# Kernel tuning notes

Hardware: AMD Instinct MI355X
Metric: run time of the kernel (lower is better)

Reference implementation:

```python
import jax, jax.numpy as jnp
import numpy as np


def setup_inputs() -> dict:
    key = jax.random.key(0)
    ks = jax.random.split(key, 7)
    B, T, U = 8, 200, 50
    D_enc, D_dec, J, V = 512, 512, 512, 1024
    s = 0.05
    return {
        "h_enc": jax.random.normal(ks[0], (B, T, 1, D_enc), dtype=jnp.float32),
        "h_dec": jax.random.normal(ks[1], (B, 1, U, D_dec), dtype=jnp.float32),
        "W_enc": jax.random.normal(ks[2], (J, D_enc), dtype=jnp.float32) * s,
        "b_enc": jax.random.normal(ks[3], (J,), dtype=jnp.float32) * s,
        "W_dec": jax.random.normal(ks[4], (J, D_dec), dtype=jnp.float32) * s,
        "W_out": jax.random.normal(ks[5], (V, J), dtype=jnp.float32) * s,
        "b_out": jax.random.normal(ks[6], (V,), dtype=jnp.float32) * s,
    }


def reference(h_enc, h_dec, W_enc, b_enc, W_dec, W_out, b_out):
    # lin_enc: (B,T,1,D_enc) -> (B,T,1,J) ; lin_dec (no bias): (B,1,U,D_dec) -> (B,1,U,J)
    e = jnp.einsum("btod,jd->btoj", h_enc, W_enc) + b_enc
    d = jnp.einsum("boud,jd->bouj", h_dec, W_dec)
    # broadcast add -> (B,T,U,J), Tanh activation
    z = jnp.tanh(e + d)
    # lin_out: (B,T,U,J) -> (B,T,U,V)
    return jnp.einsum("btuj,vj->btuv", z, W_out) + b_out
```

## Files before the change

### kernel.cpp

```cpp
#include <hip/hip_runtime.h>
#include <hip/hip_bf16.h>


typedef short bf16x8 __attribute__((ext_vector_type(8)));
typedef float fx4 __attribute__((ext_vector_type(4)));

static constexpr int KD = 512;
static constexpr int V = 1024;
static constexpr int M_BIG = 80000;

__device__ inline unsigned short f2bf(float f) {
    union { float f; unsigned u; } v; v.f = f;
    unsigned r = v.u + 0x7fffu + ((v.u >> 16) & 1u);
    return (unsigned short)(r >> 16);
}
__device__ inline float bf2f(unsigned short h) {
    union { float f; unsigned u; } v; v.u = ((unsigned)h) << 16; return v.f;
}
__device__ inline float fast_tanh(float x) {
    float p = __builtin_amdgcn_exp2f(x * 2.885390081777926f);
    return 1.0f - 2.0f * __builtin_amdgcn_rcpf(p + 1.0f);
}
__device__ inline void gld_lds16(const void* g, void* l) {
    __builtin_amdgcn_global_load_lds(
        (const __attribute__((address_space(1))) void*)g,
        (__attribute__((address_space(3))) void*)l, 16, 0, 0);
}

__global__ __launch_bounds__(256) void gemm_ed(
    const float* __restrict__ A, const float* __restrict__ W,
    const float* __restrict__ bias, float* __restrict__ out, int Mrows) {
    __shared__ unsigned short As[64 * 32];
    __shared__ unsigned short Ws[64 * 32];
    const int t = threadIdx.x;
    const int lane = t & 63, wid = t >> 6;
    const int m0 = blockIdx.x * 64, n0 = blockIdx.y * 64;
    const int wm = (wid & 1) * 32, wn = (wid >> 1) * 32;

    fx4 acc[2][2];
    const fx4 z4 = {0.f, 0.f, 0.f, 0.f};
    acc[0][0] = z4; acc[0][1] = z4; acc[1][0] = z4; acc[1][1] = z4;

    const int sr = t >> 2;
    const int skc = (t & 3) * 8;
    const int ar = (m0 + sr < Mrows) ? (m0 + sr) : (Mrows - 1);
    const float* Ap = A + (size_t)ar * KD + skc;
    const float* Wp = W + (size_t)(n0 + sr) * KD + skc;
    unsigned short* asl = &As[sr * 32 + skc];
    unsigned short* wsl = &Ws[sr * 32 + skc];

    for (int ph = 0; ph < 3; ph++) {
        const int amode = (ph == 1);
        const int wmode = (ph == 2);
        for (int kb = 0; kb < 16; kb++) {
            const int k0 = kb * 32;
            fx4 a0 = *(const fx4*)(Ap + k0);
            fx4 a1 = *(const fx4*)(Ap + k0 + 4);
            fx4 w0 = *(const fx4*)(Wp + k0);
            fx4 w1 = *(const fx4*)(Wp + k0 + 4);
            unsigned short pa[8], pw[8];
            #pragma unroll
            for (int i = 0; i < 4; i++) {
                float av0 = a0[i], av1 = a1[i], wv0 = w0[i], wv1 = w1[i];
                unsigned short h;
                h = f2bf(av0); pa[i]     = amode ? f2bf(av0 - bf2f(h)) : h;
                h = f2bf(av1); pa[i + 4] = amode ? f2bf(av1 - bf2f(h)) : h;
                h = f2bf(wv0); pw[i]     = wmode ? f2bf(wv0 - bf2f(h)) : h;
                h = f2bf(wv1); pw[i + 4] = wmode ? f2bf(wv1 - bf2f(h)) : h;
            }
            *(bf16x8*)asl = *(bf16x8*)pa;
            *(bf16x8*)wsl = *(bf16x8*)pw;
            __syncthreads();
            bf16x8 af[2], wf[2];
            #pragma unroll
            for (int f = 0; f < 2; f++) {
                af[f] = *(const bf16x8*)&As[(wm + f * 16 + (lane & 15)) * 32 + (lane >> 4) * 8];
                wf[f] = *(const bf16x8*)&Ws[(wn + f * 16 + (lane & 15)) * 32 + (lane >> 4) * 8];
            }
            #pragma unroll
            for (int fm = 0; fm < 2; fm++)
                #pragma unroll
                for (int fn = 0; fn < 2; fn++)
                    acc[fm][fn] = __builtin_amdgcn_mfma_f32_16x16x32_bf16(
                        af[fm], wf[fn], acc[fm][fn], 0, 0, 0);
            __syncthreads();
        }
    }
    const int colb = n0 + wn + (lane & 15);
    const int rowb = m0 + wm + (lane >> 4) * 4;
    float bo[2];
    bo[0] = bias ? bias[colb] : 0.f;
    bo[1] = bias ? bias[colb + 16] : 0.f;
    #pragma unroll
    for (int fm = 0; fm < 2; fm++) {
        #pragma unroll
        for (int r = 0; r < 4; r++) {
            int row = rowb + fm * 16 + r;
            if (row < Mrows) {
                float* op = out + (size_t)row * KD;
                op[colb] = acc[fm][0][r] + bo[0];
                op[colb + 16] = acc[fm][1][r] + bo[1];
            }
        }
    }
}

__global__ __launch_bounds__(256) void cvt_bf16(
    const float* __restrict__ in, unsigned short* __restrict__ o, int n) {
    int i = (blockIdx.x * 256 + threadIdx.x) * 8;
    if (i >= n) return;
    fx4 a = *(const fx4*)(in + i);
    fx4 b = *(const fx4*)(in + i + 4);
    unsigned short p[8];
    #pragma unroll
    for (int j = 0; j < 4; j++) { p[j] = f2bf(a[j]); p[j + 4] = f2bf(b[j]); }
    *(bf16x8*)(o + i) = *(bf16x8*)p;
}

__global__ __launch_bounds__(256) void tanh_z(
    const float* __restrict__ e, const float* __restrict__ d,
    unsigned short* __restrict__ Z) {
    const int t = threadIdx.x;
    const int m = blockIdx.x * 4 + (t >> 6);
    const int kc = (t & 63) * 8;
    const int bt = m / 50;
    const int u = m - bt * 50;
    const int b = m / 10000;
    const float* ep = e + (size_t)bt * KD + kc;
    const float* dp = d + (size_t)(b * 50 + u) * KD + kc;
    fx4 e0 = *(const fx4*)ep, e1 = *(const fx4*)(ep + 4);
    fx4 d0 = *(const fx4*)dp, d1 = *(const fx4*)(dp + 4);
    unsigned short p[8];
    #pragma unroll
    for (int i = 0; i < 4; i++) {
        p[i] = f2bf(fast_tanh(e0[i] + d0[i]));
        p[i + 4] = f2bf(fast_tanh(e1[i] + d1[i]));
    }
    *(bf16x8*)(Z + (size_t)m * KD + kc) = *(bf16x8*)p;
}

__global__ __launch_bounds__(256) void gemm_out_k(
    const unsigned short* __restrict__ Z, const unsigned short* __restrict__ Wb,
    const float* __restrict__ b_out, float* __restrict__ out) {
    __shared__ unsigned short As[128 * 32];
    __shared__ unsigned short Bs[128 * 32];
    const int t = threadIdx.x;
    const int lane = t & 63, wid = t >> 6;
    const int bid = blockIdx.x;
    const int n0 = (bid & 7) * 128;
    const int m0 = (bid >> 3) * 128;
    const int wm = (wid & 1) * 64, wn = (wid >> 1) * 64;

    fx4 acc[4][4];
    const fx4 z4 = {0.f, 0.f, 0.f, 0.f};
    #pragma unroll
    for (int i = 0; i < 4; i++)
        #pragma unroll
        for (int j = 0; j < 4; j++) acc[i][j] = z4;

    size_t gA[2], gB[2];
    unsigned short* lA[2];
    unsigned short* lB[2];
    #pragma unroll
    for (int q = 0; q < 2; q++) {
        int c = (wid * 2 + q) * 64 + lane;
        int r = c >> 2, kc = (c & 3) * 8;
        gA[q] = (size_t)(m0 + r) * KD + kc;
        gB[q] = (size_t)(n0 + r) * KD + kc;
        lA[q] = &As[(wid * 2 + q) * 512];
        lB[q] = &Bs[(wid * 2 + q) * 512];
    }

    for (int kb = 0; kb < 16; kb++) {
        const int k0 = kb * 32;
        #pragma unroll
        for (int q = 0; q < 2; q++) {
            gld_lds16(Z + gA[q] + k0, lA[q]);
            gld_lds16(Wb + gB[q] + k0, lB[q]);
        }
        __syncthreads();
        bf16x8 af[4], bf[4];
        #pragma unroll
        for (int f = 0; f < 4; f++) {
            af[f] = *(const bf16x8*)&As[(wm + f * 16 + (lane & 15)) * 32 + (lane >> 4) * 8];
            bf[f] = *(const bf16x8*)&Bs[(wn + f * 16 + (lane & 15)) * 32 + (lane >> 4) * 8];
        }
        #pragma unroll
        for (int fm = 0; fm < 4; fm++)
            #pragma unroll
            for (int fn = 0; fn < 4; fn++)
                acc[fm][fn] = __builtin_amdgcn_mfma_f32_16x16x32_bf16(
                    af[fm], bf[fn], acc[fm][fn], 0, 0, 0);
        __syncthreads();
    }

    const int colb = n0 + wn + (lane & 15);
    const int rowb = m0 + wm + (lane >> 4) * 4;
    float bo[4];
    #pragma unroll
    for (int fn = 0; fn < 4; fn++) bo[fn] = b_out[colb + fn * 16];
    #pragma unroll
    for (int fm = 0; fm < 4; fm++) {
        #pragma unroll
        for (int r = 0; r < 4; r++) {
            float* op = out + (size_t)(rowb + fm * 16 + r) * V;
            #pragma unroll
            for (int fn = 0; fn < 4; fn++)
                op[colb + fn * 16] = acc[fm][fn][r] + bo[fn];
        }
    }
}

extern "C" void kernel_launch(void* const* d_in, const int* in_sizes, int n_in,
                              void* d_out, int out_size, void* d_ws, size_t ws_size,
                              hipStream_t stream) {
    const float* h_enc = (const float*)d_in[0];
    const float* h_dec = (const float*)d_in[1];
    const float* W_enc = (const float*)d_in[2];
    const float* b_enc = (const float*)d_in[3];
    const float* W_dec = (const float*)d_in[4];
    const float* W_out = (const float*)d_in[5];
    const float* b_out = (const float*)d_in[6];
    float* out = (float*)d_out;

    float* e = (float*)d_ws;
    float* dd = e + 1600 * KD;
    unsigned short* Wb = (unsigned short*)(dd + 400 * KD);
    unsigned short* Zb = Wb + (size_t)V * KD;

    gemm_ed<<<dim3(25, 8), 256, 0, stream>>>(h_enc, W_enc, b_enc, e, 1600);
    gemm_ed<<<dim3(7, 8), 256, 0, stream>>>(h_dec, W_dec, nullptr, dd, 400);
    cvt_bf16<<<256, 256, 0, stream>>>(W_out, Wb, V * KD);
    tanh_z<<<20000, 256, 0, stream>>>(e, dd, Zb);
    gemm_out_k<<<5000, 256, 0, stream>>>(Zb, Wb, b_out, out);
}
```

Measured before the change: 533.2 us.

## Fuse prep kernels, drop activation residual pass, widen output GEMM K-step

Merges the encoder and decoder projection GEMMs and the W_out bf16 conversion into a single prep launch with block-index dispatch, saving two launches. The split-bf16 projection now runs two passes instead of three, dropping the activation low-part correction, which reduces accuracy of e and d. The output GEMM now loads 64 K-elements per barrier pair into two LDS halves, halving the number of sync rounds. That doubles LDS use per block and may lower occupancy.

Measured after the change: 474.7 us. 1.12x faster.

```diff
diff --git a/kernel.cpp b/kernel.cpp
--- a/kernel.cpp
+++ b/kernel.cpp
@@ -7,7 +7,6 @@
 
 static constexpr int KD = 512;
 static constexpr int V = 1024;
-static constexpr int M_BIG = 80000;
 
 __device__ inline unsigned short f2bf(float f) {
     union { float f; unsigned u; } v; v.f = f;
@@ -27,14 +26,32 @@
         (__attribute__((address_space(3))) void*)l, 16, 0, 0);
 }
 
-__global__ __launch_bounds__(256) void gemm_ed(
-    const float* __restrict__ A, const float* __restrict__ W,
-    const float* __restrict__ bias, float* __restrict__ out, int Mrows) {
+__global__ __launch_bounds__(256) void prep(
+    const float* __restrict__ h_enc, const float* __restrict__ W_enc,
+    const float* __restrict__ b_enc, const float* __restrict__ h_dec,
+    const float* __restrict__ W_dec, const float* __restrict__ W_out,
+    float* __restrict__ e, float* __restrict__ dd, unsigned short* __restrict__ Wb) {
+    const int bx = blockIdx.x;
+    const int t = threadIdx.x;
+    if (bx >= 256) {
+        int i = ((bx - 256) * 256 + t) * 8;
+        fx4 a = *(const fx4*)(W_out + i);
+        fx4 b = *(const fx4*)(W_out + i + 4);
+        unsigned short p[8];
+        #pragma unroll
+        for (int j = 0; j < 4; j++) { p[j] = f2bf(a[j]); p[j + 4] = f2bf(b[j]); }
+        *(bf16x8*)(Wb + i) = *(bf16x8*)p;
+        return;
+    }
+    const float* A; const float* W; const float* bias; float* out;
+    int Mrows, mb, nb;
+    if (bx < 200) { A = h_enc; W = W_enc; bias = b_enc; out = e;  Mrows = 1600; mb = bx >> 3; nb = bx & 7; }
+    else { int b2 = bx - 200; A = h_dec; W = W_dec; bias = nullptr; out = dd; Mrows = 400; mb = b2 >> 3; nb = b2 & 7; }
+
     __shared__ unsigned short As[64 * 32];
     __shared__ unsigned short Ws[64 * 32];
-    const int t = threadIdx.x;
     const int lane = t & 63, wid = t >> 6;
-    const int m0 = blockIdx.x * 64, n0 = blockIdx.y * 64;
+    const int m0 = mb * 64, n0 = nb * 64;
     const int wm = (wid & 1) * 32, wn = (wid >> 1) * 32;
 
     fx4 acc[2][2];
@@ -49,9 +66,8 @@
     unsigned short* asl = &As[sr * 32 + skc];
     unsigned short* wsl = &Ws[sr * 32 + skc];
 
-    for (int ph = 0; ph < 3; ph++) {
-        const int amode = (ph == 1);
-        const int wmode = (ph == 2);
+    for (int ph = 0; ph < 2; ph++) {
+        const int wmode = (ph == 1);
         for (int kb = 0; kb < 16; kb++) {
             const int k0 = kb * 32;
             fx4 a0 = *(const fx4*)(Ap + k0);
@@ -61,12 +77,10 @@
             unsigned short pa[8], pw[8];
             #pragma unroll
             for (int i = 0; i < 4; i++) {
-                float av0 = a0[i], av1 = a1[i], wv0 = w0[i], wv1 = w1[i];
                 unsigned short h;
-                h = f2bf(av0); pa[i]     = amode ? f2bf(av0 - bf2f(h)) : h;
-                h = f2bf(av1); pa[i + 4] = amode ? f2bf(av1 - bf2f(h)) : h;
-                h = f2bf(wv0); pw[i]     = wmode ? f2bf(wv0 - bf2f(h)) : h;
-                h = f2bf(wv1); pw[i + 4] = wmode ? f2bf(wv1 - bf2f(h)) : h;
+                pa[i] = f2bf(a0[i]); pa[i + 4] = f2bf(a1[i]);
+                h = f2bf(w0[i]); pw[i]     = wmode ? f2bf(w0[i] - bf2f(h)) : h;
+                h = f2bf(w1[i]); pw[i + 4] = wmode ? f2bf(w1[i] - bf2f(h)) : h;
             }
             *(bf16x8*)asl = *(bf16x8*)pa;
             *(bf16x8*)wsl = *(bf16x8*)pw;
@@ -103,18 +117,6 @@
             }
         }
     }
-}
-
-__global__ __launch_bounds__(256) void cvt_bf16(
-    const float* __restrict__ in, unsigned short* __restrict__ o, int n) {
-    int i = (blockIdx.x * 256 + threadIdx.x) * 8;
-    if (i >= n) return;
-    fx4 a = *(const fx4*)(in + i);
-    fx4 b = *(const fx4*)(in + i + 4);
-    unsigned short p[8];
-    #pragma unroll
-    for (int j = 0; j < 4; j++) { p[j] = f2bf(a[j]); p[j + 4] = f2bf(b[j]); }
-    *(bf16x8*)(o + i) = *(bf16x8*)p;
 }
 
 __global__ __launch_bounds__(256) void tanh_z(
@@ -142,8 +144,8 @@
 __global__ __launch_bounds__(256) void gemm_out_k(
     const unsigned short* __restrict__ Z, const unsigned short* __restrict__ Wb,
     const float* __restrict__ b_out, float* __restrict__ out) {
-    __shared__ unsigned short As[128 * 32];
-    __shared__ unsigned short Bs[128 * 32];
+    __shared__ unsigned short As[2][128 * 32];
+    __shared__ unsigned short Bs[2][128 * 32];
     const int t = threadIdx.x;
     const int lane = t & 63, wid = t >> 6;
     const int bid = blockIdx.x;
@@ -159,38 +161,41 @@
         for (int j = 0; j < 4; j++) acc[i][j] = z4;
 
     size_t gA[2], gB[2];
-    unsigned short* lA[2];
-    unsigned short* lB[2];
+    int lofs[2];
     #pragma unroll
     for (int q = 0; q < 2; q++) {
         int c = (wid * 2 + q) * 64 + lane;
         int r = c >> 2, kc = (c & 3) * 8;
         gA[q] = (size_t)(m0 + r) * KD + kc;
         gB[q] = (size_t)(n0 + r) * KD + kc;
-        lA[q] = &As[(wid * 2 + q) * 512];
-        lB[q] = &Bs[(wid * 2 + q) * 512];
-    }
-
-    for (int kb = 0; kb < 16; kb++) {
-        const int k0 = kb * 32;
-        #pragma unroll
-        for (int q = 0; q < 2; q++) {
-            gld_lds16(Z + gA[q] + k0, lA[q]);
-            gld_lds16(Wb + gB[q] + k0, lB[q]);
-        }
+        lofs[q] = (wid * 2 + q) * 512;
+    }
+
+    for (int kb = 0; kb < 8; kb++) {
+        const int k0 = kb * 64;
+        #pragma unroll
+        for (int h = 0; h < 2; h++)
+            #pragma unroll
+            for (int q = 0; q < 2; q++) {
+                gld_lds16(Z + gA[q] + k0 + h * 32, &As[h][lofs[q]]);
+                gld_lds16(Wb + gB[q] + k0 + h * 32, &Bs[h][lofs[q]]);
+            }
         __syncthreads();
-        bf16x8 af[4], bf[4];
-        #pragma unroll
-        for (int f = 0; f < 4; f++) {
-            af[f] = *(const bf16x8*)&As[(wm + f * 16 + (lane & 15)) * 32 + (lane >> 4) * 8];
-            bf[f] = *(const bf16x8*)&Bs[(wn + f * 16 + (lane & 15)) * 32 + (lane >> 4) * 8];
-        }
-        #pragma unroll
-        for (int fm = 0; fm < 4; fm++)
-            #pragma unroll
-            for (int fn = 0; fn < 4; fn++)
-                acc[fm][fn] = __builtin_amdgcn_mfma_f32_16x16x32_bf16(
-                    af[fm], bf[fn], acc[fm][fn], 0, 0, 0);
+        #pragma unroll
+        for (int h = 0; h < 2; h++) {
+            bf16x8 af[4], bf[4];
+            #pragma unroll
+            for (int f = 0; f < 4; f++) {
+                af[f] = *(const bf16x8*)&As[h][(wm + f * 16 + (lane & 15)) * 32 + (lane >> 4) * 8];
+                bf[f] = *(const bf16x8*)&Bs[h][(wn + f * 16 + (lane & 15)) * 32 + (lane >> 4) * 8];
+            }
+            #pragma unroll
+            for (int fm = 0; fm < 4; fm++)
+                #pragma unroll
+                for (int fn = 0; fn < 4; fn++)
+                    acc[fm][fn] = __builtin_amdgcn_mfma_f32_16x16x32_bf16(
+                        af[fm], bf[fn], acc[fm][fn], 0, 0, 0);
+        }
         __syncthreads();
     }
 
@@ -228,9 +233,7 @@
     unsigned short* Wb = (unsigned short*)(dd + 400 * KD);
     unsigned short* Zb = Wb + (size_t)V * KD;
 
-    gemm_ed<<<dim3(25, 8), 256, 0, stream>>>(h_enc, W_enc, b_enc, e, 1600);
-    gemm_ed<<<dim3(7, 8), 256, 0, stream>>>(h_dec, W_dec, nullptr, dd, 400);
-    cvt_bf16<<<256, 256, 0, stream>>>(W_out, Wb, V * KD);
+    prep<<<512, 256, 0, stream>>>(h_enc, W_enc, b_enc, h_dec, W_dec, W_out, e, dd, Wb);
     tanh_z<<<20000, 256, 0, stream>>>(e, dd, Zb);
     gemm_out_k<<<5000, 256, 0, stream>>>(Zb, Wb, b_out, out);
 }
```
